# Performance work log

Hardware: AMD Instinct MI355X
Metric: run time of the kernel (lower is better)

## Reference

```python
import jax, jax.numpy as jnp
import numpy as np

B, S, E, H, D = 4, 2048, 1024, 16, 64

def setup_inputs() -> dict:
    key = jax.random.key(0)
    ks = jax.random.split(key, 9)
    sc = 0.02
    return {
        "x":  jax.random.normal(ks[0], (B, S, E), jnp.float32),
        "Wq": jax.random.normal(ks[1], (H, E, D), jnp.float32) * sc,
        "bq": jax.random.normal(ks[2], (H, D), jnp.float32) * sc,
        "Wk": jax.random.normal(ks[3], (H, E, D), jnp.float32) * sc,
        "bk": jax.random.normal(ks[4], (H, D), jnp.float32) * sc,
        "Wv": jax.random.normal(ks[5], (H, E, D), jnp.float32) * sc,
        "bv": jax.random.normal(ks[6], (H, D), jnp.float32) * sc,
        "Wp": jax.random.normal(ks[7], (H * D, E), jnp.float32) * sc,
        "bp": jax.random.normal(ks[8], (E,), jnp.float32) * sc,
    }

def reference(x, Wq, bq, Wk, bk, Wv, bv, Wp, bp):
    # Per-head projections (stacked): [B,S,E] x [H,E,D] -> [B,H,S,D]
    q = jnp.einsum('bse,hed->bhsd', x, Wq) + bq[None, :, None, :]
    k = jnp.einsum('bse,hed->bhsd', x, Wk) + bk[None, :, None, :]
    v = jnp.einsum('bse,hed->bhsd', x, Wv) + bv[None, :, None, :]
    # Scaled scores with causal mask: [B,H,S,S]
    scores = jnp.einsum('bhqd,bhkd->bhqk', q, k) / jnp.sqrt(jnp.float32(D))
    causal = jnp.tril(jnp.ones((S, S), dtype=bool))
    scores = jnp.where(causal[None, None], scores, -jnp.inf)
    attn = jax.nn.softmax(scores, axis=-1)
    out = jnp.einsum('bhqk,bhkd->bhqd', attn, v)          # [B,H,S,D]
    out = out.transpose(0, 2, 1, 3).reshape(B, S, H * D)  # concat heads
    return out @ Wp + bp                                   # [B,S,E]
```

## Files before the change

### kernel.cpp

```cpp
#include <hip/hip_runtime.h>
#include <hip/hip_bf16.h>

#define B_ 4
#define S_ 2048
#define E_ 1024
#define H_ 16
#define D_ 64
#define QSCALE 0.18033688011112042f

typedef __attribute__((ext_vector_type(8))) short bf16x8;
typedef __attribute__((ext_vector_type(4))) float f32x4;

__device__ __forceinline__ f32x4 mfma16(bf16x8 a, bf16x8 b, f32x4 c) {
    return __builtin_amdgcn_mfma_f32_16x16x32_bf16(a, b, c, 0, 0, 0);
}
__device__ __forceinline__ short f2bs(float f) {
    __hip_bfloat16 h = __float2bfloat16(f);
    return *reinterpret_cast<short*>(&h);
}

__global__ __launch_bounds__(256) void conv_wqkv(
    const float* __restrict__ Wq, const float* __restrict__ Wk,
    const float* __restrict__ Wv, short* __restrict__ WT)
{
    const int mat = blockIdx.x >> 4;
    const int kt  = blockIdx.x & 15;
    const int which = mat >> 4, h = mat & 15;
    const float* src = (which == 0 ? Wq : which == 1 ? Wk : Wv) + (size_t)h * E_ * D_;
    __shared__ float T[64][65];
    const int tid = threadIdx.x;
    const int k0 = kt * 64;
    #pragma unroll
    for (int it = 0; it < 4; ++it) {
        int lin = tid + it * 256;
        int kr = lin >> 4, dc = (lin & 15) * 4;
        const float4 v = *(const float4*)&src[(size_t)(k0 + kr) * D_ + dc];
        T[kr][dc] = v.x; T[kr][dc + 1] = v.y; T[kr][dc + 2] = v.z; T[kr][dc + 3] = v.w;
    }
    __syncthreads();
    #pragma unroll
    for (int it = 0; it < 4; ++it) {
        int lin = tid + it * 256;
        int dr = lin >> 4, kc = (lin & 15) * 4;
        ushort4 o;
        o.x = (unsigned short)f2bs(T[kc][dr]);
        o.y = (unsigned short)f2bs(T[kc + 1][dr]);
        o.z = (unsigned short)f2bs(T[kc + 2][dr]);
        o.w = (unsigned short)f2bs(T[kc + 3][dr]);
        *(ushort4*)&WT[((size_t)mat * 64 + dr) * E_ + k0 + kc] = o;
    }
}

__global__ __launch_bounds__(256) void conv_wp(
    const float* __restrict__ Wp, short* __restrict__ WpT)
{
    const int ktile = blockIdx.x & 15, ntile = blockIdx.x >> 4;
    const int k0 = ktile * 64, n0 = ntile * 64;
    __shared__ float T[64][65];
    const int tid = threadIdx.x;
    #pragma unroll
    for (int it = 0; it < 4; ++it) {
        int lin = tid + it * 256;
        int kr = lin >> 4, nc = (lin & 15) * 4;
        const float4 v = *(const float4*)&Wp[(size_t)(k0 + kr) * E_ + n0 + nc];
        T[kr][nc] = v.x; T[kr][nc + 1] = v.y; T[kr][nc + 2] = v.z; T[kr][nc + 3] = v.w;
    }
    __syncthreads();
    #pragma unroll
    for (int it = 0; it < 4; ++it) {
        int lin = tid + it * 256;
        int nr = lin >> 4, kc = (lin & 15) * 4;
        ushort4 o;
        o.x = (unsigned short)f2bs(T[kc][nr]);
        o.y = (unsigned short)f2bs(T[kc + 1][nr]);
        o.z = (unsigned short)f2bs(T[kc + 2][nr]);
        o.w = (unsigned short)f2bs(T[kc + 3][nr]);
        *(ushort4*)&WpT[(size_t)(n0 + nr) * E_ + k0 + kc] = o;
    }
}

__global__ __launch_bounds__(256, 2) void qkv_fused(
    const float* __restrict__ x, const short* __restrict__ WT,
    const float* __restrict__ bq, const float* __restrict__ bk,
    const float* __restrict__ bv,
    short* __restrict__ Qw, short* __restrict__ Kw, short* __restrict__ VTw)
{
    const int h = blockIdx.y;
    const int m0 = blockIdx.x * 128;
    __shared__ short Xs[128 * 72];
    __shared__ short Wt3[3][64 * 72];

    const int tid = threadIdx.x;
    const int lane = tid & 63, w = tid >> 6;
    const int l15 = lane & 15, qd = lane >> 4;

    f32x4 zero = {0.f, 0.f, 0.f, 0.f};
    f32x4 acc[3][2][4];
    #pragma unroll
    for (int a = 0; a < 3; ++a)
        #pragma unroll
        for (int b = 0; b < 2; ++b)
            #pragma unroll
            for (int c = 0; c < 4; ++c) acc[a][b][c] = zero;

    float4 xr[4][2];
    bf16x8 wr[6];

    #pragma unroll
    for (int it = 0; it < 4; ++it) {
        int lin = tid + it * 256;
        int row = lin >> 3, cb = (lin & 7) * 8;
        xr[it][0] = *(const float4*)&x[(size_t)(m0 + row) * E_ + cb];
        xr[it][1] = *(const float4*)&x[(size_t)(m0 + row) * E_ + cb + 4];
    }
    #pragma unroll
    for (int it = 0; it < 6; ++it) {
        int lin = tid + it * 256;
        int mat = lin >> 9, rem = lin & 511;
        int d = rem >> 3, cb = (rem & 7) * 8;
        wr[it] = *(const bf16x8*)&WT[((size_t)(mat * 16 + h) * 64 + d) * E_ + cb];
    }

    for (int k0 = 0; k0 < E_; k0 += 64) {
        #pragma unroll
        for (int it = 0; it < 4; ++it) {
            int lin = tid + it * 256;
            int row = lin >> 3, cb = (lin & 7) * 8;
            bf16x8 pk;
            pk[0] = f2bs(xr[it][0].x); pk[1] = f2bs(xr[it][0].y);
            pk[2] = f2bs(xr[it][0].z); pk[3] = f2bs(xr[it][0].w);
            pk[4] = f2bs(xr[it][1].x); pk[5] = f2bs(xr[it][1].y);
            pk[6] = f2bs(xr[it][1].z); pk[7] = f2bs(xr[it][1].w);
            *(bf16x8*)&Xs[row * 72 + cb] = pk;
        }
        #pragma unroll
        for (int it = 0; it < 6; ++it) {
            int lin = tid + it * 256;
            int mat = lin >> 9, rem = lin & 511;
            int d = rem >> 3, cb = (rem & 7) * 8;
            *(bf16x8*)&Wt3[mat][d * 72 + cb] = wr[it];
        }
        __syncthreads();
        if (k0 + 64 < E_) {
            #pragma unroll
            for (int it = 0; it < 4; ++it) {
                int lin = tid + it * 256;
                int row = lin >> 3, cb = (lin & 7) * 8;
                xr[it][0] = *(const float4*)&x[(size_t)(m0 + row) * E_ + k0 + 64 + cb];
                xr[it][1] = *(const float4*)&x[(size_t)(m0 + row) * E_ + k0 + 64 + cb + 4];
            }
            #pragma unroll
            for (int it = 0; it < 6; ++it) {
                int lin = tid + it * 256;
                int mat = lin >> 9, rem = lin & 511;
                int d = rem >> 3, cb = (rem & 7) * 8;
                wr[it] = *(const bf16x8*)&WT[((size_t)(mat * 16 + h) * 64 + d) * E_ + k0 + 64 + cb];
            }
        }
        #pragma unroll
        for (int t = 0; t < 2; ++t) {
            bf16x8 am0 = *(const bf16x8*)&Xs[(w * 32 + l15) * 72 + t * 32 + qd * 8];
            bf16x8 am1 = *(const bf16x8*)&Xs[(w * 32 + 16 + l15) * 72 + t * 32 + qd * 8];
            #pragma unroll
            for (int mat = 0; mat < 3; ++mat)
                #pragma unroll
                for (int c = 0; c < 4; ++c) {
                    bf16x8 bb = *(const bf16x8*)&Wt3[mat][(c * 16 + l15) * 72 + t * 32 + qd * 8];
                    acc[mat][0][c] = mfma16(am0, bb, acc[mat][0][c]);
                    acc[mat][1][c] = mfma16(am1, bb, acc[mat][1][c]);
                }
        }
        __syncthreads();
    }

    const int bb = m0 >> 11;
    const int s0 = m0 & (S_ - 1);
    float bqv[4], bkv[4], bvv[4];
    #pragma unroll
    for (int c = 0; c < 4; ++c) {
        int d = c * 16 + l15;
        bqv[c] = bq[h * D_ + d];
        bkv[c] = bk[h * D_ + d];
        bvv[c] = bv[h * D_ + d];
    }
    #pragma unroll
    for (int mi = 0; mi < 2; ++mi)
        #pragma unroll
        for (int c = 0; c < 4; ++c)
            #pragma unroll
            for (int r = 0; r < 4; ++r) {
                int s = s0 + w * 32 + mi * 16 + qd * 4 + r;
                size_t base = (((size_t)bb * H_ + h) * S_ + s) * D_ + c * 16 + l15;
                Qw[base] = f2bs((acc[0][mi][c][r] + bqv[c]) * QSCALE);
                Kw[base] = f2bs(acc[1][mi][c][r] + bkv[c]);
            }
    short* ep = Xs + w * (32 * 66);
    #pragma unroll
    for (int mi = 0; mi < 2; ++mi)
        #pragma unroll
        for (int c = 0; c < 4; ++c)
            #pragma unroll
            for (int r = 0; r < 4; ++r)
                ep[(mi * 16 + qd * 4 + r) * 66 + c * 16 + l15] =
                    f2bs(acc[2][mi][c][r] + bvv[c]);
    asm volatile("s_waitcnt lgkmcnt(0)" ::: "memory");
    const int sr = lane & 31, dh = lane >> 5;
    const size_t vbase = ((size_t)bb * H_ + h) * (size_t)D_ * S_;
    #pragma unroll
    for (int it = 0; it < 32; ++it) {
        int dd = it * 2 + dh;
        VTw[vbase + (size_t)dd * S_ + s0 + w * 32 + sr] = ep[sr * 66 + dd];
    }
}

__global__ __launch_bounds__(256, 2) void attn(
    const short* __restrict__ Qw, const short* __restrict__ Kw,
    const short* __restrict__ VTw, short* __restrict__ Ow)
{
    const int jj = blockIdx.x;
    const int bh = blockIdx.y;
    const int b = bh >> 4, h = bh & 15;
    const size_t kbase = ((size_t)b * H_ + h) * (size_t)S_ * D_;
    const size_t vbase = ((size_t)b * H_ + h) * (size_t)D_ * S_;

    __shared__ short Qs[128 * 72];
    __shared__ short Ks[2][64 * 72];
    __shared__ short Vt[2][64 * 72];

    const int tid = threadIdx.x;
    const int lane = tid & 63, w = tid >> 6;
    const int l15 = lane & 15, qd = lane >> 4;

    const int r0s = tid >> 3;
    const int c0s = (tid & 7) * 8;
    const int r1s = r0s + 32;

    #pragma unroll
    for (int phase = 0; phase < 2; ++phase) {
        const int qt = phase ? jj : (15 - jj);

        #pragma unroll
        for (int it = 0; it < 4; ++it) {
            int row = w * 32 + it * 8 + (lane >> 3);
            int cb = (lane & 7) * 8;
            *(bf16x8*)&Qs[row * 72 + cb] =
                *(const bf16x8*)&Qw[kbase + (size_t)(qt * 128 + row) * D_ + cb];
        }
        asm volatile("s_waitcnt lgkmcnt(0)" ::: "memory");
        bf16x8 qf[2][2];
        #pragma unroll
        for (int mi = 0; mi < 2; ++mi)
            #pragma unroll
            for (int t = 0; t < 2; ++t)
                qf[mi][t] = *(const bf16x8*)&Qs[(w * 32 + mi * 16 + l15) * 72 + t * 32 + qd * 8];

        f32x4 zero = {0.f, 0.f, 0.f, 0.f};
        f32x4 oacc[2][4];
        float lrow[2][4];
        #pragma unroll
        for (int mi = 0; mi < 2; ++mi) {
            #pragma unroll
            for (int c = 0; c < 4; ++c) oacc[mi][c] = zero;
            #pragma unroll
            for (int r = 0; r < 4; ++r) lrow[mi][r] = 0.f;
        }

        const int nkt = (qt + 1) * 2;
        bf16x8 kr0, kr1, vr0, vr1;
        kr0 = *(const bf16x8*)&Kw[kbase + (size_t)r0s * D_ + c0s];
        kr1 = *(const bf16x8*)&Kw[kbase + (size_t)r1s * D_ + c0s];
        vr0 = *(const bf16x8*)&VTw[vbase + (size_t)r0s * S_ + c0s];
        vr1 = *(const bf16x8*)&VTw[vbase + (size_t)r1s * S_ + c0s];
        *(bf16x8*)&Ks[0][r0s * 72 + c0s] = kr0;
        *(bf16x8*)&Ks[0][r1s * 72 + c0s] = kr1;
        *(bf16x8*)&Vt[0][r0s * 72 + c0s] = vr0;
        *(bf16x8*)&Vt[0][r1s * 72 + c0s] = vr1;
        __syncthreads();

        int p = 0;
        for (int kt = 0; kt < nkt; ++kt) {
            const bool pre = (kt + 1 < nkt);
            if (pre) {
                kr0 = *(const bf16x8*)&Kw[kbase + (size_t)((kt + 1) * 64 + r0s) * D_ + c0s];
                kr1 = *(const bf16x8*)&Kw[kbase + (size_t)((kt + 1) * 64 + r1s) * D_ + c0s];
                vr0 = *(const bf16x8*)&VTw[vbase + (size_t)r0s * S_ + (kt + 1) * 64 + c0s];
                vr1 = *(const bf16x8*)&VTw[vbase + (size_t)r1s * S_ + (kt + 1) * 64 + c0s];
            }
            f32x4 sc[2][4];
            #pragma unroll
            for (int mi = 0; mi < 2; ++mi)
                #pragma unroll
                for (int c = 0; c < 4; ++c) sc[mi][c] = zero;
            #pragma unroll
            for (int t = 0; t < 2; ++t)
                #pragma unroll
                for (int c = 0; c < 4; ++c) {
                    bf16x8 bk = *(const bf16x8*)&Ks[p][(c * 16 + l15) * 72 + t * 32 + qd * 8];
                    sc[0][c] = mfma16(qf[0][t], bk, sc[0][c]);
                    sc[1][c] = mfma16(qf[1][t], bk, sc[1][c]);
                }
            #pragma unroll
            for (int mi = 0; mi < 2; ++mi) {
                const int fr = qt * 128 + w * 32 + mi * 16;
                if (kt * 64 + 63 > fr) {
                    #pragma unroll
                    for (int c = 0; c < 4; ++c) {
                        int col = kt * 64 + c * 16 + l15;
                        #pragma unroll
                        for (int r = 0; r < 4; ++r)
                            if (col > fr + qd * 4 + r) sc[mi][c][r] = -1e30f;
                    }
                }
                #pragma unroll
                for (int c = 0; c < 4; ++c)
                    #pragma unroll
                    for (int r = 0; r < 4; ++r) {
                        float pv = __builtin_amdgcn_exp2f(sc[mi][c][r]);
                        lrow[mi][r] += pv;
                        Qs[(w * 32 + mi * 16 + qd * 4 + r) * 72 + c * 16 + l15] = f2bs(pv);
                    }
            }
            asm volatile("s_waitcnt lgkmcnt(0)" ::: "memory");
            #pragma unroll
            for (int t = 0; t < 2; ++t) {
                bf16x8 ap0 = *(const bf16x8*)&Qs[(w * 32 + l15) * 72 + t * 32 + qd * 8];
                bf16x8 ap1 = *(const bf16x8*)&Qs[(w * 32 + 16 + l15) * 72 + t * 32 + qd * 8];
                #pragma unroll
                for (int c = 0; c < 4; ++c) {
                    bf16x8 bv = *(const bf16x8*)&Vt[p][(c * 16 + l15) * 72 + t * 32 + qd * 8];
                    oacc[0][c] = mfma16(ap0, bv, oacc[0][c]);
                    oacc[1][c] = mfma16(ap1, bv, oacc[1][c]);
                }
            }
            if (pre) {
                *(bf16x8*)&Ks[1 - p][r0s * 72 + c0s] = kr0;
                *(bf16x8*)&Ks[1 - p][r1s * 72 + c0s] = kr1;
                *(bf16x8*)&Vt[1 - p][r0s * 72 + c0s] = vr0;
                *(bf16x8*)&Vt[1 - p][r1s * 72 + c0s] = vr1;
            }
            __syncthreads();
            p ^= 1;
        }

        #pragma unroll
        for (int mi = 0; mi < 2; ++mi) {
            float inv[4];
            #pragma unroll
            for (int r = 0; r < 4; ++r) {
                float l = lrow[mi][r];
                l += __shfl_xor(l, 1);
                l += __shfl_xor(l, 2);
                l += __shfl_xor(l, 4);
                l += __shfl_xor(l, 8);
                inv[r] = 1.f / l;
            }
            #pragma unroll
            for (int c = 0; c < 4; ++c)
                #pragma unroll
                for (int r = 0; r < 4; ++r) {
                    int s = qt * 128 + w * 32 + mi * 16 + qd * 4 + r;
                    Ow[((size_t)b * S_ + s) * (H_ * D_) + h * D_ + c * 16 + l15] =
                        f2bs(oacc[mi][c][r] * inv[r]);
                }
        }
    }
}

__global__ __launch_bounds__(256, 3) void out_proj(
    const short* __restrict__ Oin, const short* __restrict__ WpT,
    const float* __restrict__ bp, float* __restrict__ out)
{
    const int m0 = blockIdx.x * 128;
    const int n0 = blockIdx.y * 64;
    __shared__ short As[128 * 72];
    __shared__ short Bs[64 * 72];
    const int tid = threadIdx.x;
    const int lane = tid & 63, w = tid >> 6;
    const int l15 = lane & 15, qd = lane >> 4;

    f32x4 zero = {0.f, 0.f, 0.f, 0.f};
    f32x4 acc[2][4];
    #pragma unroll
    for (int mi = 0; mi < 2; ++mi)
        #pragma unroll
        for (int c = 0; c < 4; ++c) acc[mi][c] = zero;

    bf16x8 ar[4], br[2];
    #pragma unroll
    for (int it = 0; it < 4; ++it) {
        int lin = tid + it * 256;
        int row = lin >> 3, cb = (lin & 7) * 8;
        ar[it] = *(const bf16x8*)&Oin[(size_t)(m0 + row) * E_ + cb];
    }
    #pragma unroll
    for (int it = 0; it < 2; ++it) {
        int lin = tid + it * 256;
        int row = lin >> 3, cb = (lin & 7) * 8;
        br[it] = *(const bf16x8*)&WpT[(size_t)(n0 + row) * E_ + cb];
    }

    for (int k0 = 0; k0 < E_; k0 += 64) {
        #pragma unroll
        for (int it = 0; it < 4; ++it) {
            int lin = tid + it * 256;
            int row = lin >> 3, cb = (lin & 7) * 8;
            *(bf16x8*)&As[row * 72 + cb] = ar[it];
        }
        #pragma unroll
        for (int it = 0; it < 2; ++it) {
            int lin = tid + it * 256;
            int row = lin >> 3, cb = (lin & 7) * 8;
            *(bf16x8*)&Bs[row * 72 + cb] = br[it];
        }
        __syncthreads();
        if (k0 + 64 < E_) {
            #pragma unroll
            for (int it = 0; it < 4; ++it) {
                int lin = tid + it * 256;
                int row = lin >> 3, cb = (lin & 7) * 8;
                ar[it] = *(const bf16x8*)&Oin[(size_t)(m0 + row) * E_ + k0 + 64 + cb];
            }
            #pragma unroll
            for (int it = 0; it < 2; ++it) {
                int lin = tid + it * 256;
                int row = lin >> 3, cb = (lin & 7) * 8;
                br[it] = *(const bf16x8*)&WpT[(size_t)(n0 + row) * E_ + k0 + 64 + cb];
            }
        }
        #pragma unroll
        for (int t = 0; t < 2; ++t) {
            bf16x8 a0 = *(const bf16x8*)&As[(w * 32 + l15) * 72 + t * 32 + qd * 8];
            bf16x8 a1 = *(const bf16x8*)&As[(w * 32 + 16 + l15) * 72 + t * 32 + qd * 8];
            #pragma unroll
            for (int c = 0; c < 4; ++c) {
                bf16x8 bb = *(const bf16x8*)&Bs[(c * 16 + l15) * 72 + t * 32 + qd * 8];
                acc[0][c] = mfma16(a0, bb, acc[0][c]);
                acc[1][c] = mfma16(a1, bb, acc[1][c]);
            }
        }
        __syncthreads();
    }
    #pragma unroll
    for (int mi = 0; mi < 2; ++mi)
        #pragma unroll
        for (int c = 0; c < 4; ++c) {
            float bpv = bp[n0 + c * 16 + l15];
            #pragma unroll
            for (int r = 0; r < 4; ++r) {
                int m = m0 + w * 32 + mi * 16 + qd * 4 + r;
                out[(size_t)m * E_ + n0 + c * 16 + l15] = acc[mi][c][r] + bpv;
            }
        }
}

extern "C" void kernel_launch(void* const* d_in, const int* in_sizes, int n_in,
                              void* d_out, int out_size, void* d_ws, size_t ws_size,
                              hipStream_t stream)
{
    const float* x  = (const float*)d_in[0];
    const float* Wq = (const float*)d_in[1];
    const float* bq = (const float*)d_in[2];
    const float* Wk = (const float*)d_in[3];
    const float* bk = (const float*)d_in[4];
    const float* Wv = (const float*)d_in[5];
    const float* bv = (const float*)d_in[6];
    const float* Wp = (const float*)d_in[7];
    const float* bp = (const float*)d_in[8];
    float* out = (float*)d_out;

    const size_t nQKV = (size_t)B_ * H_ * S_ * D_;
    short* Qw   = (short*)d_ws;
    short* Kw   = Qw + nQKV;
    short* VTw  = Kw + nQKV;
    short* buf3 = VTw + nQKV;
    short* WT   = buf3;
    short* Ow   = buf3;
    short* WpT  = Qw;

    conv_wqkv<<<dim3(768), 256, 0, stream>>>(Wq, Wk, Wv, WT);
    qkv_fused<<<dim3(64, 16), 256, 0, stream>>>(x, WT, bq, bk, bv, Qw, Kw, VTw);
    attn<<<dim3(8, 64), 256, 0, stream>>>(Qw, Kw, VTw, Ow);
    conv_wp<<<dim3(256), 256, 0, stream>>>(Wp, WpT);
    out_proj<<<dim3(64, 16), 256, 0, stream>>>(Ow, WpT, bp, out);
}
```

Before: 261.4 us.

## Use direct global-to-LDS loads and larger tiles across QKV, attention, out-proj

Replaces the register-staged global-to-shared copies in qkv_fused, attn and out_proj with global_load_lds direct-to-LDS transfers into a swizzled 8-row sub-block layout, double-buffered. qkv_fused doubles its M tile to 256 rows, with each wave converting its own x rows and a 32-wide K step. out_proj grows to 128x128 tiles with 4x4 MFMA accumulators per wave. attn reads Q fragments straight from global and raises occupancy to 3 blocks. The intent is to cut register pressure and VGPR round-trips for staging and to raise MFMA reuse per LDS read. It risks a larger register footprint, fewer blocks for the GEMMs, and per-wave x conversion without a block-wide barrier.

```diff
diff --git a/kernel.cpp b/kernel.cpp
--- a/kernel.cpp
+++ b/kernel.cpp
@@ -17,6 +17,15 @@
 __device__ __forceinline__ short f2bs(float f) {
     __hip_bfloat16 h = __float2bfloat16(f);
     return *reinterpret_cast<short*>(&h);
+}
+__device__ __forceinline__ void glds16(const void* gptr, void* lptr) {
+    __builtin_amdgcn_global_load_lds(
+        (const __attribute__((address_space(1))) unsigned int*)(unsigned long long)gptr,
+        (__attribute__((address_space(3))) unsigned int*)(unsigned int)(unsigned long long)lptr,
+        16, 0, 0);
+}
+__device__ __forceinline__ int sbi(int r, int cshort) {
+    return (r >> 3) * 520 + (r & 7) * 64 + cshort;
 }
 
 __global__ __launch_bounds__(256) void conv_wqkv(
@@ -86,91 +95,71 @@
     short* __restrict__ Qw, short* __restrict__ Kw, short* __restrict__ VTw)
 {
     const int h = blockIdx.y;
-    const int m0 = blockIdx.x * 128;
-    __shared__ short Xs[128 * 72];
-    __shared__ short Wt3[3][64 * 72];
+    const int m0 = blockIdx.x * 256;
+    __shared__ short Xs[4 * 64 * 72];
+    __shared__ short Wt3[2][3 * 2080];
 
     const int tid = threadIdx.x;
     const int lane = tid & 63, w = tid >> 6;
     const int l15 = lane & 15, qd = lane >> 4;
 
     f32x4 zero = {0.f, 0.f, 0.f, 0.f};
-    f32x4 acc[3][2][4];
+    f32x4 acc[3][4][4];
     #pragma unroll
     for (int a = 0; a < 3; ++a)
         #pragma unroll
-        for (int b = 0; b < 2; ++b)
+        for (int b = 0; b < 4; ++b)
             #pragma unroll
             for (int c = 0; c < 4; ++c) acc[a][b][c] = zero;
 
-    float4 xr[4][2];
-    bf16x8 wr[6];
-
-    #pragma unroll
-    for (int it = 0; it < 4; ++it) {
-        int lin = tid + it * 256;
-        int row = lin >> 3, cb = (lin & 7) * 8;
-        xr[it][0] = *(const float4*)&x[(size_t)(m0 + row) * E_ + cb];
-        xr[it][1] = *(const float4*)&x[(size_t)(m0 + row) * E_ + cb + 4];
-    }
-    #pragma unroll
-    for (int it = 0; it < 6; ++it) {
-        int lin = tid + it * 256;
-        int mat = lin >> 9, rem = lin & 511;
-        int d = rem >> 3, cb = (rem & 7) * 8;
-        wr[it] = *(const bf16x8*)&WT[((size_t)(mat * 16 + h) * 64 + d) * E_ + cb];
-    }
-
-    for (int k0 = 0; k0 < E_; k0 += 64) {
-        #pragma unroll
-        for (int it = 0; it < 4; ++it) {
-            int lin = tid + it * 256;
-            int row = lin >> 3, cb = (lin & 7) * 8;
+    #pragma unroll
+    for (int i = 0; i < 3; ++i) {
+        int lin = w * 3 + i, mt = lin >> 2, s = lin & 3;
+        glds16(&WT[((size_t)(mt * 16 + h) * 64 + s * 16 + (lane >> 2)) * E_ + (lane & 3) * 8],
+               &Wt3[0][mt * 2080 + s * 520]);
+    }
+    __syncthreads();
+
+    short* xw = &Xs[w * 4608];
+    const float* xrowb = &x[(size_t)(m0 + w * 64 + lane) * E_];
+    int p = 0;
+    for (int k0 = 0; k0 < E_; k0 += 32) {
+        if (k0 + 32 < E_) {
+            #pragma unroll
+            for (int i = 0; i < 3; ++i) {
+                int lin = w * 3 + i, mt = lin >> 2, s = lin & 3;
+                glds16(&WT[((size_t)(mt * 16 + h) * 64 + s * 16 + (lane >> 2)) * E_ + k0 + 32 + (lane & 3) * 8],
+                       &Wt3[p ^ 1][mt * 2080 + s * 520]);
+            }
+        }
+        float4 xv[8];
+        #pragma unroll
+        for (int j = 0; j < 8; ++j) xv[j] = *(const float4*)&xrowb[k0 + j * 4];
+        #pragma unroll
+        for (int j = 0; j < 4; ++j) {
             bf16x8 pk;
-            pk[0] = f2bs(xr[it][0].x); pk[1] = f2bs(xr[it][0].y);
-            pk[2] = f2bs(xr[it][0].z); pk[3] = f2bs(xr[it][0].w);
-            pk[4] = f2bs(xr[it][1].x); pk[5] = f2bs(xr[it][1].y);
-            pk[6] = f2bs(xr[it][1].z); pk[7] = f2bs(xr[it][1].w);
-            *(bf16x8*)&Xs[row * 72 + cb] = pk;
-        }
-        #pragma unroll
-        for (int it = 0; it < 6; ++it) {
-            int lin = tid + it * 256;
-            int mat = lin >> 9, rem = lin & 511;
-            int d = rem >> 3, cb = (rem & 7) * 8;
-            *(bf16x8*)&Wt3[mat][d * 72 + cb] = wr[it];
-        }
+            pk[0] = f2bs(xv[2 * j].x);     pk[1] = f2bs(xv[2 * j].y);
+            pk[2] = f2bs(xv[2 * j].z);     pk[3] = f2bs(xv[2 * j].w);
+            pk[4] = f2bs(xv[2 * j + 1].x); pk[5] = f2bs(xv[2 * j + 1].y);
+            pk[6] = f2bs(xv[2 * j + 1].z); pk[7] = f2bs(xv[2 * j + 1].w);
+            *(bf16x8*)&xw[lane * 72 + j * 8] = pk;
+        }
+        asm volatile("s_waitcnt lgkmcnt(0)" ::: "memory");
+        bf16x8 a[4];
+        #pragma unroll
+        for (int mi = 0; mi < 4; ++mi)
+            a[mi] = *(const bf16x8*)&xw[(mi * 16 + l15) * 72 + qd * 8];
+        #pragma unroll
+        for (int mt = 0; mt < 3; ++mt)
+            #pragma unroll
+            for (int c = 0; c < 4; ++c) {
+                bf16x8 bb = *(const bf16x8*)&Wt3[p][mt * 2080 + c * 520 + l15 * 32 + qd * 8];
+                #pragma unroll
+                for (int mi = 0; mi < 4; ++mi)
+                    acc[mt][mi][c] = mfma16(a[mi], bb, acc[mt][mi][c]);
+            }
         __syncthreads();
-        if (k0 + 64 < E_) {
-            #pragma unroll
-            for (int it = 0; it < 4; ++it) {
-                int lin = tid + it * 256;
-                int row = lin >> 3, cb = (lin & 7) * 8;
-                xr[it][0] = *(const float4*)&x[(size_t)(m0 + row) * E_ + k0 + 64 + cb];
-                xr[it][1] = *(const float4*)&x[(size_t)(m0 + row) * E_ + k0 + 64 + cb + 4];
-            }
-            #pragma unroll
-            for (int it = 0; it < 6; ++it) {
-                int lin = tid + it * 256;
-                int mat = lin >> 9, rem = lin & 511;
-                int d = rem >> 3, cb = (rem & 7) * 8;
-                wr[it] = *(const bf16x8*)&WT[((size_t)(mat * 16 + h) * 64 + d) * E_ + k0 + 64 + cb];
-            }
-        }
-        #pragma unroll
-        for (int t = 0; t < 2; ++t) {
-            bf16x8 am0 = *(const bf16x8*)&Xs[(w * 32 + l15) * 72 + t * 32 + qd * 8];
-            bf16x8 am1 = *(const bf16x8*)&Xs[(w * 32 + 16 + l15) * 72 + t * 32 + qd * 8];
-            #pragma unroll
-            for (int mat = 0; mat < 3; ++mat)
-                #pragma unroll
-                for (int c = 0; c < 4; ++c) {
-                    bf16x8 bb = *(const bf16x8*)&Wt3[mat][(c * 16 + l15) * 72 + t * 32 + qd * 8];
-                    acc[mat][0][c] = mfma16(am0, bb, acc[mat][0][c]);
-                    acc[mat][1][c] = mfma16(am1, bb, acc[mat][1][c]);
-                }
-        }
-        __syncthreads();
+        p ^= 1;
     }
 
     const int bb = m0 >> 11;
@@ -184,19 +173,19 @@
         bvv[c] = bv[h * D_ + d];
     }
     #pragma unroll
-    for (int mi = 0; mi < 2; ++mi)
+    for (int mi = 0; mi < 4; ++mi)
         #pragma unroll
         for (int c = 0; c < 4; ++c)
             #pragma unroll
             for (int r = 0; r < 4; ++r) {
-                int s = s0 + w * 32 + mi * 16 + qd * 4 + r;
+                int s = s0 + w * 64 + mi * 16 + qd * 4 + r;
                 size_t base = (((size_t)bb * H_ + h) * S_ + s) * D_ + c * 16 + l15;
                 Qw[base] = f2bs((acc[0][mi][c][r] + bqv[c]) * QSCALE);
                 Kw[base] = f2bs(acc[1][mi][c][r] + bkv[c]);
             }
-    short* ep = Xs + w * (32 * 66);
-    #pragma unroll
-    for (int mi = 0; mi < 2; ++mi)
+    short* ep = xw;
+    #pragma unroll
+    for (int mi = 0; mi < 4; ++mi)
         #pragma unroll
         for (int c = 0; c < 4; ++c)
             #pragma unroll
@@ -207,13 +196,15 @@
     const int sr = lane & 31, dh = lane >> 5;
     const size_t vbase = ((size_t)bb * H_ + h) * (size_t)D_ * S_;
     #pragma unroll
-    for (int it = 0; it < 32; ++it) {
-        int dd = it * 2 + dh;
-        VTw[vbase + (size_t)dd * S_ + s0 + w * 32 + sr] = ep[sr * 66 + dd];
-    }
-}
-
-__global__ __launch_bounds__(256, 2) void attn(
+    for (int it = 0; it < 64; ++it) {
+        int half = it >> 5;
+        int dd = (it & 31) * 2 + dh;
+        int sr2 = half * 32 + sr;
+        VTw[vbase + (size_t)dd * S_ + s0 + w * 64 + sr2] = ep[sr2 * 66 + dd];
+    }
+}
+
+__global__ __launch_bounds__(256, 3) void attn(
     const short* __restrict__ Qw, const short* __restrict__ Kw,
     const short* __restrict__ VTw, short* __restrict__ Ow)
 {
@@ -223,36 +214,26 @@
     const size_t kbase = ((size_t)b * H_ + h) * (size_t)S_ * D_;
     const size_t vbase = ((size_t)b * H_ + h) * (size_t)D_ * S_;
 
-    __shared__ short Qs[128 * 72];
-    __shared__ short Ks[2][64 * 72];
-    __shared__ short Vt[2][64 * 72];
+    __shared__ short Ps[128 * 72];
+    __shared__ short Ks[2][8 * 520];
+    __shared__ short Vt[2][8 * 520];
 
     const int tid = threadIdx.x;
     const int lane = tid & 63, w = tid >> 6;
     const int l15 = lane & 15, qd = lane >> 4;
-
-    const int r0s = tid >> 3;
-    const int c0s = (tid & 7) * 8;
-    const int r1s = r0s + 32;
+    const int gr = lane >> 3, gc = (lane & 7) * 8;
 
     #pragma unroll
     for (int phase = 0; phase < 2; ++phase) {
         const int qt = phase ? jj : (15 - jj);
 
-        #pragma unroll
-        for (int it = 0; it < 4; ++it) {
-            int row = w * 32 + it * 8 + (lane >> 3);
-            int cb = (lane & 7) * 8;
-            *(bf16x8*)&Qs[row * 72 + cb] =
-                *(const bf16x8*)&Qw[kbase + (size_t)(qt * 128 + row) * D_ + cb];
-        }
-        asm volatile("s_waitcnt lgkmcnt(0)" ::: "memory");
         bf16x8 qf[2][2];
         #pragma unroll
         for (int mi = 0; mi < 2; ++mi)
             #pragma unroll
             for (int t = 0; t < 2; ++t)
-                qf[mi][t] = *(const bf16x8*)&Qs[(w * 32 + mi * 16 + l15) * 72 + t * 32 + qd * 8];
+                qf[mi][t] = *(const bf16x8*)&Qw[kbase +
+                    (size_t)(qt * 128 + w * 32 + mi * 16 + l15) * D_ + t * 32 + qd * 8];
 
         f32x4 zero = {0.f, 0.f, 0.f, 0.f};
         f32x4 oacc[2][4];
@@ -266,25 +247,25 @@
         }
 
         const int nkt = (qt + 1) * 2;
-        bf16x8 kr0, kr1, vr0, vr1;
-        kr0 = *(const bf16x8*)&Kw[kbase + (size_t)r0s * D_ + c0s];
-        kr1 = *(const bf16x8*)&Kw[kbase + (size_t)r1s * D_ + c0s];
-        vr0 = *(const bf16x8*)&VTw[vbase + (size_t)r0s * S_ + c0s];
-        vr1 = *(const bf16x8*)&VTw[vbase + (size_t)r1s * S_ + c0s];
-        *(bf16x8*)&Ks[0][r0s * 72 + c0s] = kr0;
-        *(bf16x8*)&Ks[0][r1s * 72 + c0s] = kr1;
-        *(bf16x8*)&Vt[0][r0s * 72 + c0s] = vr0;
-        *(bf16x8*)&Vt[0][r1s * 72 + c0s] = vr1;
+        #pragma unroll
+        for (int i = 0; i < 2; ++i) {
+            int sb = w * 2 + i;
+            glds16(&Kw[kbase + (size_t)(sb * 8 + gr) * D_ + gc], &Ks[0][sb * 520]);
+            glds16(&VTw[vbase + (size_t)(sb * 8 + gr) * S_ + gc], &Vt[0][sb * 520]);
+        }
         __syncthreads();
 
         int p = 0;
         for (int kt = 0; kt < nkt; ++kt) {
-            const bool pre = (kt + 1 < nkt);
-            if (pre) {
-                kr0 = *(const bf16x8*)&Kw[kbase + (size_t)((kt + 1) * 64 + r0s) * D_ + c0s];
-                kr1 = *(const bf16x8*)&Kw[kbase + (size_t)((kt + 1) * 64 + r1s) * D_ + c0s];
-                vr0 = *(const bf16x8*)&VTw[vbase + (size_t)r0s * S_ + (kt + 1) * 64 + c0s];
-                vr1 = *(const bf16x8*)&VTw[vbase + (size_t)r1s * S_ + (kt + 1) * 64 + c0s];
+            if (kt + 1 < nkt) {
+                #pragma unroll
+                for (int i = 0; i < 2; ++i) {
+                    int sb = w * 2 + i;
+                    glds16(&Kw[kbase + (size_t)((kt + 1) * 64 + sb * 8 + gr) * D_ + gc],
+                           &Ks[p ^ 1][sb * 520]);
+                    glds16(&VTw[vbase + (size_t)(sb * 8 + gr) * S_ + (kt + 1) * 64 + gc],
+                           &Vt[p ^ 1][sb * 520]);
+                }
             }
             f32x4 sc[2][4];
             #pragma unroll
@@ -295,7 +276,7 @@
             for (int t = 0; t < 2; ++t)
                 #pragma unroll
                 for (int c = 0; c < 4; ++c) {
-                    bf16x8 bk = *(const bf16x8*)&Ks[p][(c * 16 + l15) * 72 + t * 32 + qd * 8];
+                    bf16x8 bk = *(const bf16x8*)&Ks[p][sbi(c * 16 + l15, t * 32 + qd * 8)];
                     sc[0][c] = mfma16(qf[0][t], bk, sc[0][c]);
                     sc[1][c] = mfma16(qf[1][t], bk, sc[1][c]);
                 }
@@ -317,26 +298,20 @@
                     for (int r = 0; r < 4; ++r) {
                         float pv = __builtin_amdgcn_exp2f(sc[mi][c][r]);
                         lrow[mi][r] += pv;
-                        Qs[(w * 32 + mi * 16 + qd * 4 + r) * 72 + c * 16 + l15] = f2bs(pv);
+                        Ps[(w * 32 + mi * 16 + qd * 4 + r) * 72 + c * 16 + l15] = f2bs(pv);
                     }
             }
             asm volatile("s_waitcnt lgkmcnt(0)" ::: "memory");
             #pragma unroll
             for (int t = 0; t < 2; ++t) {
-                bf16x8 ap0 = *(const bf16x8*)&Qs[(w * 32 + l15) * 72 + t * 32 + qd * 8];
-                bf16x8 ap1 = *(const bf16x8*)&Qs[(w * 32 + 16 + l15) * 72 + t * 32 + qd * 8];
+                bf16x8 ap0 = *(const bf16x8*)&Ps[(w * 32 + l15) * 72 + t * 32 + qd * 8];
+                bf16x8 ap1 = *(const bf16x8*)&Ps[(w * 32 + 16 + l15) * 72 + t * 32 + qd * 8];
                 #pragma unroll
                 for (int c = 0; c < 4; ++c) {
-                    bf16x8 bv = *(const bf16x8*)&Vt[p][(c * 16 + l15) * 72 + t * 32 + qd * 8];
+                    bf16x8 bv = *(const bf16x8*)&Vt[p][sbi(c * 16 + l15, t * 32 + qd * 8)];
                     oacc[0][c] = mfma16(ap0, bv, oacc[0][c]);
                     oacc[1][c] = mfma16(ap1, bv, oacc[1][c]);
                 }
-            }
-            if (pre) {
-                *(bf16x8*)&Ks[1 - p][r0s * 72 + c0s] = kr0;
-                *(bf16x8*)&Ks[1 - p][r1s * 72 + c0s] = kr1;
-                *(bf16x8*)&Vt[1 - p][r0s * 72 + c0s] = vr0;
-                *(bf16x8*)&Vt[1 - p][r1s * 72 + c0s] = vr1;
             }
             __syncthreads();
             p ^= 1;
@@ -366,91 +341,80 @@
     }
 }
 
-__global__ __launch_bounds__(256, 3) void out_proj(
+__global__ __launch_bounds__(256, 2) void out_proj(
     const short* __restrict__ Oin, const short* __restrict__ WpT,
     const float* __restrict__ bp, float* __restrict__ out)
 {
     const int m0 = blockIdx.x * 128;
-    const int n0 = blockIdx.y * 64;
-    __shared__ short As[128 * 72];
-    __shared__ short Bs[64 * 72];
+    const int n0 = blockIdx.y * 128;
+    __shared__ short As[2][16 * 520];
+    __shared__ short Bs[2][16 * 520];
+
     const int tid = threadIdx.x;
     const int lane = tid & 63, w = tid >> 6;
     const int l15 = lane & 15, qd = lane >> 4;
+    const int gr = lane >> 3, gc = (lane & 7) * 8;
+    const int mh = (w & 1) * 64, nh = (w >> 1) * 64;
 
     f32x4 zero = {0.f, 0.f, 0.f, 0.f};
-    f32x4 acc[2][4];
-    #pragma unroll
-    for (int mi = 0; mi < 2; ++mi)
+    f32x4 acc[4][4];
+    #pragma unroll
+    for (int mi = 0; mi < 4; ++mi)
         #pragma unroll
         for (int c = 0; c < 4; ++c) acc[mi][c] = zero;
 
-    bf16x8 ar[4], br[2];
-    #pragma unroll
-    for (int it = 0; it < 4; ++it) {
-        int lin = tid + it * 256;
-        int row = lin >> 3, cb = (lin & 7) * 8;
-        ar[it] = *(const bf16x8*)&Oin[(size_t)(m0 + row) * E_ + cb];
-    }
-    #pragma unroll
-    for (int it = 0; it < 2; ++it) {
-        int lin = tid + it * 256;
-        int row = lin >> 3, cb = (lin & 7) * 8;
-        br[it] = *(const bf16x8*)&WpT[(size_t)(n0 + row) * E_ + cb];
-    }
-
+    #pragma unroll
+    for (int i = 0; i < 8; ++i) {
+        int lin = w * 8 + i;
+        if (lin < 16)
+            glds16(&Oin[(size_t)(m0 + lin * 8 + gr) * E_ + gc], &As[0][lin * 520]);
+        else
+            glds16(&WpT[(size_t)(n0 + (lin - 16) * 8 + gr) * E_ + gc], &Bs[0][(lin - 16) * 520]);
+    }
+    __syncthreads();
+
+    int p = 0;
     for (int k0 = 0; k0 < E_; k0 += 64) {
-        #pragma unroll
-        for (int it = 0; it < 4; ++it) {
-            int lin = tid + it * 256;
-            int row = lin >> 3, cb = (lin & 7) * 8;
-            *(bf16x8*)&As[row * 72 + cb] = ar[it];
-        }
-        #pragma unroll
-        for (int it = 0; it < 2; ++it) {
-            int lin = tid + it * 256;
-            int row = lin >> 3, cb = (lin & 7) * 8;
-            *(bf16x8*)&Bs[row * 72 + cb] = br[it];
+        if (k0 + 64 < E_) {
+            #pragma unroll
+            for (int i = 0; i < 8; ++i) {
+                int lin = w * 8 + i;
+                if (lin < 16)
+                    glds16(&Oin[(size_t)(m0 + lin * 8 + gr) * E_ + k0 + 64 + gc],
+                           &As[p ^ 1][lin * 520]);
+                else
+                    glds16(&WpT[(size_t)(n0 + (lin - 16) * 8 + gr) * E_ + k0 + 64 + gc],
+                           &Bs[p ^ 1][(lin - 16) * 520]);
+            }
+        }
+        #pragma unroll
+        for (int t = 0; t < 2; ++t) {
+            bf16x8 a[4];
+            #pragma unroll
+            for (int mi = 0; mi < 4; ++mi)
+                a[mi] = *(const bf16x8*)&As[p][sbi(mh + mi * 16 + l15, t * 32 + qd * 8)];
+            #pragma unroll
+            for (int c = 0; c < 4; ++c) {
+                bf16x8 bb = *(const bf16x8*)&Bs[p][sbi(nh + c * 16 + l15, t * 32 + qd * 8)];
+                #pragma unroll
+                for (int mi = 0; mi < 4; ++mi)
+                    acc[mi][c] = mfma16(a[mi], bb, acc[mi][c]);
+            }
         }
         __syncthreads();
-        if (k0 + 64 < E_) {
-            #pragma unroll
-            for (int it = 0; it < 4; ++it) {
-                int lin = tid + it * 256;
-                int row = lin >> 3, cb = (lin & 7) * 8;
-                ar[it] = *(const bf16x8*)&Oin[(size_t)(m0 + row) * E_ + k0 + 64 + cb];
-            }
-            #pragma unroll
-            for (int it = 0; it < 2; ++it) {
-                int lin = tid + it * 256;
-                int row = lin >> 3, cb = (lin & 7) * 8;
-                br[it] = *(const bf16x8*)&WpT[(size_t)(n0 + row) * E_ + k0 + 64 + cb];
-            }
-        }
-        #pragma unroll
-        for (int t = 0; t < 2; ++t) {
-            bf16x8 a0 = *(const bf16x8*)&As[(w * 32 + l15) * 72 + t * 32 + qd * 8];
-            bf16x8 a1 = *(const bf16x8*)&As[(w * 32 + 16 + l15) * 72 + t * 32 + qd * 8];
-            #pragma unroll
-            for (int c = 0; c < 4; ++c) {
-                bf16x8 bb = *(const bf16x8*)&Bs[(c * 16 + l15) * 72 + t * 32 + qd * 8];
-                acc[0][c] = mfma16(a0, bb, acc[0][c]);
-                acc[1][c] = mfma16(a1, bb, acc[1][c]);
-            }
-        }
-        __syncthreads();
-    }
-    #pragma unroll
-    for (int mi = 0; mi < 2; ++mi)
-        #pragma unroll
-        for (int c = 0; c < 4; ++c) {
-            float bpv = bp[n0 + c * 16 + l15];
+        p ^= 1;
+    }
+    #pragma unroll
+    for (int c = 0; c < 4; ++c) {
+        float bpv = bp[n0 + nh + c * 16 + l15];
+        #pragma unroll
+        for (int mi = 0; mi < 4; ++mi)
             #pragma unroll
             for (int r = 0; r < 4; ++r) {
-                int m = m0 + w * 32 + mi * 16 + qd * 4 + r;
-                out[(size_t)m * E_ + n0 + c * 16 + l15] = acc[mi][c][r] + bpv;
-            }
-        }
+                int m = m0 + mh + mi * 16 + qd * 4 + r;
+                out[(size_t)m * E_ + n0 + nh + c * 16 + l15] = acc[mi][c][r] + bpv;
+            }
+    }
 }
 
 extern "C" void kernel_launch(void* const* d_in, const int* in_sizes, int n_in,
@@ -478,8 +442,8 @@
     short* WpT  = Qw;
 
     conv_wqkv<<<dim3(768), 256, 0, stream>>>(Wq, Wk, Wv, WT);
-    qkv_fused<<<dim3(64, 16), 256, 0, stream>>>(x, WT, bq, bk, bv, Qw, Kw, VTw);
+    qkv_fused<<<dim3(32, 16), 256, 0, stream>>>(x, WT, bq, bk, bv, Qw, Kw, VTw);
     attn<<<dim3(8, 64), 256, 0, stream>>>(Qw, Kw, VTw, Ow);
     conv_wp<<<dim3(256), 256, 0, stream>>>(Wp, WpT);
-    out_proj<<<dim3(64, 16), 256, 0, stream>>>(Ow, WpT, bp, out);
-}
+    out_proj<<<dim3(64, 8), 256, 0, stream>>>(Ow, WpT, bp, out);
+}
```

New measurement: 280.4 us. 1.07x slower.
